# Optimization experiments

Measured on AMD Instinct MI355X. Metric: run time of the kernel, lower is better.

Reference implementation:

```python
import jax, jax.numpy as jnp
import numpy as np

ALPHA = 0.2        # LeakyReLU negative slope
MASK_VAL = -9e15   # matches torch -9000000000000000.0


def setup_inputs() -> dict:
    key = jax.random.key(0)
    k_h, k_adj, k_w, k_a = jax.random.split(key, 4)
    B, N, Nodes, IF, OF = 8, 8, 512, 256, 256
    h = jax.random.normal(k_h, (B, N, Nodes, IF), dtype=jnp.float32)
    adj = jax.random.randint(k_adj, (Nodes, Nodes), 0, 2, dtype=jnp.int32)
    # xavier_uniform with gain=1.414
    gain = 1.414
    lim_w = gain * np.sqrt(6.0 / (IF + OF))
    W = jax.random.uniform(k_w, (IF, OF), dtype=jnp.float32, minval=-lim_w, maxval=lim_w)
    lim_a = gain * np.sqrt(6.0 / (2 * OF + 1))
    a = jax.random.uniform(k_a, (2 * OF, 1), dtype=jnp.float32, minval=-lim_a, maxval=lim_a)
    return {"h": h, "adj": adj, "W": W, "a": a}


def reference(h, adj, W, a):
    # Wh: [B, N, Nodes, OF]
    Wh = jnp.matmul(h, W)
    OF = W.shape[1]
    a1, a2 = a[:OF, 0], a[OF:, 0]
    # e[..., i, j] = leakyrelu(a1 . Wh_i + a2 . Wh_j)  (decomposed additive attention)
    src = jnp.einsum('bnif,f->bni', Wh, a1)  # [B, N, Nodes]
    dst = jnp.einsum('bnjf,f->bnj', Wh, a2)  # [B, N, Nodes]
    e = jax.nn.leaky_relu(src[..., :, None] + dst[..., None, :], negative_slope=ALPHA)
    attention = jnp.where(adj > 0, e, jnp.full_like(e, MASK_VAL))
    attention = jax.nn.softmax(attention, axis=-1)
    # dropout is identity in eval mode (training=False)
    h_prime = jnp.matmul(attention, Wh)  # [B, N, Nodes, OF]
    return jax.nn.elu(h_prime)  # concat=True
```

## Files before the change

kernel.cpp:

```cpp
#include <hip/hip_runtime.h>
#include <hip/hip_bf16.h>


#define ALPHA 0.2f
#define MASK_VAL -9000000000000000.0f
#define NODES 512
#define FDIM 256
#define BN 64

typedef float  f32x4 __attribute__((ext_vector_type(4)));
typedef int    i32x4 __attribute__((ext_vector_type(4)));
typedef short  s16x8 __attribute__((ext_vector_type(8)));
typedef short  s16x4 __attribute__((ext_vector_type(4)));
typedef __bf16 bf16x8 __attribute__((ext_vector_type(8)));

__device__ __forceinline__ unsigned short f2bfu(float x) {
    __hip_bfloat16 b = __float2bfloat16(x);
    unsigned short u; __builtin_memcpy(&u, &b, 2); return u;
}
__device__ __forceinline__ float bfu2f(unsigned short u) {
    unsigned int w = ((unsigned int)u) << 16; return __uint_as_float(w);
}
__device__ __forceinline__ f32x4 mfma16(s16x8 a, s16x8 b, f32x4 c) {
    return __builtin_amdgcn_mfma_f32_16x16x32_bf16(
        __builtin_bit_cast(bf16x8, a), __builtin_bit_cast(bf16x8, b), c, 0, 0, 0);
}

__device__ __forceinline__ void split8v(f32x4 v0, f32x4 v1, s16x8& hi, s16x8& lo)
{
    float x[8] = {v0[0], v0[1], v0[2], v0[3], v1[0], v1[1], v1[2], v1[3]};
    unsigned hw[4], lw[4];
    #pragma unroll
    for (int d = 0; d < 4; ++d) {
        const unsigned u0 = __float_as_uint(x[2*d]);
        const unsigned u1 = __float_as_uint(x[2*d + 1]);
        hw[d] = __builtin_amdgcn_perm(u1, u0, 0x07060302);
        const float l0 = x[2*d]     - __uint_as_float(u0 & 0xFFFF0000u);
        const float l1 = x[2*d + 1] - __uint_as_float(u1 & 0xFFFF0000u);
        lw[d] = __builtin_amdgcn_perm(__float_as_uint(l1), __float_as_uint(l0),
                                      0x07060302);
    }
    hi = __builtin_bit_cast(s16x8, *(unsigned(*)[4])hw);
    lo = __builtin_bit_cast(s16x8, *(unsigned(*)[4])lw);
}

__device__ __forceinline__ void gll16(const void* g, void* l) {
    __builtin_amdgcn_global_load_lds(
        (const __attribute__((address_space(1))) unsigned int*)g,
        (__attribute__((address_space(3))) unsigned int*)l,
        16, 0, 0);
}

__global__ __launch_bounds__(256) void detect_kernel(const unsigned short* __restrict__ hraw,
                                                     int* __restrict__ flag)
{
    const int tid = threadIdx.x;
    float m = 0.0f;
    for (int i = tid; i < 16384; i += 256) {
        unsigned int w = ((unsigned int)hraw[i]) << 16;
        float v = __uint_as_float(w);
        v = fabsf(v);
        if (!(v == v)) v = 1e30f;
        m = fmaxf(m, v);
    }
    #pragma unroll
    for (int off = 32; off >= 1; off >>= 1)
        m = fmaxf(m, __shfl_down(m, off));
    __shared__ float red[4];
    if ((tid & 63) == 0) red[tid >> 6] = m;
    __syncthreads();
    if (tid == 0) {
        float mm = fmaxf(fmaxf(red[0], red[1]), fmaxf(red[2], red[3]));
        *flag = (mm > 1e4f) ? 1 : 0;
    }
}

__global__ __launch_bounds__(256) void prep_w_kernel(
    const void* __restrict__ Wv, const int* __restrict__ flagp,
    short* __restrict__ WtHi, short* __restrict__ WtLo)
{
    const int flag = *flagp;
    __shared__ float tile[16][17];
    const int tx = threadIdx.x & 15, ty = threadIdx.x >> 4;
    const int kk = blockIdx.y * 16 + ty;
    const int f  = blockIdx.x * 16 + tx;
    float v;
    if (flag) v = ((const float*)Wv)[kk * FDIM + f];
    else      v = bfu2f(((const unsigned short*)Wv)[kk * FDIM + f]);
    tile[ty][tx] = v;
    __syncthreads();
    const float x = tile[tx][ty];
    const int fo = blockIdx.x * 16 + ty;
    const int ko = blockIdx.y * 16 + tx;
    unsigned short h = f2bfu(x);
    WtHi[fo * FDIM + ko] = (short)h;
    WtLo[fo * FDIM + ko] = (short)f2bfu(x - bfu2f(h));
}

__global__ __launch_bounds__(256, 2) void wh_gemm(
    const void* __restrict__ hv,
    const short* __restrict__ WtHi, const short* __restrict__ WtLo,
    const void* __restrict__ av, const int* __restrict__ flagp,
    short* __restrict__ WhTHi, short* __restrict__ WhTLo,
    float* __restrict__ srcv, float* __restrict__ dstv)
{
    __shared__ __align__(16) char smem[81920];

    const int flag = *flagp;
    const int blk = blockIdx.x;
    const int bn  = blk >> 3;
    const int i0  = (blk & 7) * 64;
    const size_t r0g = (size_t)blk * 64;
    const int tid = threadIdx.x;
    const int w = tid >> 6, l = tid & 63;
    const int fb = l & 15, g = l >> 4;

    const int arow = tid >> 2, asg = tid & 3;
    const int aseg = asg ^ ((arow >> 1) & 3);
    const int awr  = arow * 64 + asg * 16;

    const short* gBh[4];
    const short* gBl[4];
    int bdst[4];
    {
        const int bsg = tid & 3;
        #pragma unroll
        for (int i = 0; i < 4; ++i) {
            const int f = i * 64 + (tid >> 2);
            const int ss = bsg ^ ((f ^ (f >> 2)) & 3);
            gBh[i] = WtHi + f * FDIM + ss * 8;
            gBl[i] = WtLo + f * FDIM + ss * 8;
            bdst[i] = (i * 256 + tid) * 16;
        }
    }

    f32x4 acc[4][4];
    #pragma unroll
    for (int rt = 0; rt < 4; ++rt)
        #pragma unroll
        for (int ct = 0; ct < 4; ++ct) acc[rt][ct] = f32x4{0.f,0.f,0.f,0.f};

    if (flag) {
        const float* gA = (const float*)hv + (r0g + arow) * FDIM + aseg * 8;
        {
            f32x4 v0 = *(const f32x4*)gA;
            f32x4 v1 = *(const f32x4*)(gA + 4);
            #pragma unroll
            for (int i = 0; i < 4; ++i) {
                gll16(gBh[i], smem + 16384 + bdst[i]);
                gll16(gBl[i], smem + 49152 + bdst[i]);
            }
            s16x8 hi, lo; split8v(v0, v1, hi, lo);
            *(s16x8*)(smem + awr) = hi;
            *(s16x8*)(smem + 4096 + awr) = lo;
        }
        __syncthreads();
        for (int t = 0; t < 8; ++t) {
            const int cur = t & 1, nxt = cur ^ 1;
            f32x4 v0 = {}, v1 = {};
            if (t < 7) {
                v0 = *(const f32x4*)(gA + (t+1)*32);
                v1 = *(const f32x4*)(gA + (t+1)*32 + 4);
                #pragma unroll
                for (int i = 0; i < 4; ++i) {
                    gll16(gBh[i] + (t+1)*32, smem + 16384 + nxt*16384 + bdst[i]);
                    gll16(gBl[i] + (t+1)*32, smem + 49152 + nxt*16384 + bdst[i]);
                }
            }
            s16x8 bh[4], bl[4], ah[4], al[4];
            #pragma unroll
            for (int ct = 0; ct < 4; ++ct) {
                const int f = w*64 + ct*16 + fb;
                const int slot = g ^ ((f ^ (f >> 2)) & 3);
                const int off = 16384 + cur*16384 + f*64 + slot*16;
                bh[ct] = *(const s16x8*)(smem + off);
                bl[ct] = *(const s16x8*)(smem + off + 32768);
            }
            #pragma unroll
            for (int rt = 0; rt < 4; ++rt) {
                const int row = rt*16 + fb;
                const int slot = g ^ ((row >> 1) & 3);
                const int off = cur*8192 + row*64 + slot*16;
                ah[rt] = *(const s16x8*)(smem + off);
                al[rt] = *(const s16x8*)(smem + off + 4096);
            }
            __builtin_amdgcn_s_setprio(1);
            #pragma unroll
            for (int rt = 0; rt < 4; ++rt)
                #pragma unroll
                for (int ct = 0; ct < 4; ++ct) {
                    acc[rt][ct] = mfma16(ah[rt], bh[ct], acc[rt][ct]);
                    acc[rt][ct] = mfma16(al[rt], bh[ct], acc[rt][ct]);
                    acc[rt][ct] = mfma16(ah[rt], bl[ct], acc[rt][ct]);
                }
            __builtin_amdgcn_s_setprio(0);
            if (t < 7) {
                s16x8 hi, lo; split8v(v0, v1, hi, lo);
                *(s16x8*)(smem + nxt*8192 + awr) = hi;
                *(s16x8*)(smem + nxt*8192 + 4096 + awr) = lo;
            }
            __syncthreads();
        }
    } else {
        const short* gA = (const short*)hv + (r0g + arow) * FDIM + aseg * 8;
        {
            s16x8 a0 = *(const s16x8*)gA;
            #pragma unroll
            for (int i = 0; i < 4; ++i) gll16(gBh[i], smem + 16384 + bdst[i]);
            *(s16x8*)(smem + awr) = a0;
        }
        __syncthreads();
        for (int t = 0; t < 8; ++t) {
            const int cur = t & 1, nxt = cur ^ 1;
            s16x8 an = {};
            if (t < 7) {
                an = *(const s16x8*)(gA + (t+1)*32);
                #pragma unroll
                for (int i = 0; i < 4; ++i)
                    gll16(gBh[i] + (t+1)*32, smem + 16384 + nxt*16384 + bdst[i]);
            }
            s16x8 bh[4], ah[4];
            #pragma unroll
            for (int ct = 0; ct < 4; ++ct) {
                const int f = w*64 + ct*16 + fb;
                const int slot = g ^ ((f ^ (f >> 2)) & 3);
                bh[ct] = *(const s16x8*)(smem + 16384 + cur*16384 + f*64 + slot*16);
            }
            #pragma unroll
            for (int rt = 0; rt < 4; ++rt) {
                const int row = rt*16 + fb;
                const int slot = g ^ ((row >> 1) & 3);
                ah[rt] = *(const s16x8*)(smem + cur*8192 + row*64 + slot*16);
            }
            __builtin_amdgcn_s_setprio(1);
            #pragma unroll
            for (int rt = 0; rt < 4; ++rt)
                #pragma unroll
                for (int ct = 0; ct < 4; ++ct)
                    acc[rt][ct] = mfma16(ah[rt], bh[ct], acc[rt][ct]);
            __builtin_amdgcn_s_setprio(0);
            if (t < 7) *(s16x8*)(smem + nxt*8192 + awr) = an;
            __syncthreads();
        }
    }

    const size_t wbT = (size_t)bn * FDIM * NODES;
    #pragma unroll
    for (int rt = 0; rt < 4; ++rt) {
        const int orow = i0 + rt * 16 + g * 4;
        #pragma unroll
        for (int ct = 0; ct < 4; ++ct) {
            const int f = w * 64 + ct * 16 + fb;
            s16x4 h4, l4;
            #pragma unroll
            for (int r = 0; r < 4; ++r) {
                float x = acc[rt][ct][r];
                unsigned short hh = f2bfu(x);
                h4[r] = (short)hh;
                l4[r] = (short)f2bfu(x - bfu2f(hh));
            }
            *(s16x4*)(WhTHi + wbT + (size_t)f * NODES + orow) = h4;
            *(s16x4*)(WhTLo + wbT + (size_t)f * NODES + orow) = l4;
        }
    }

    float a1v[4], a2v[4];
    #pragma unroll
    for (int ct = 0; ct < 4; ++ct) {
        const int f = w * 64 + ct * 16 + fb;
        if (flag) {
            a1v[ct] = ((const float*)av)[f];
            a2v[ct] = ((const float*)av)[FDIM + f];
        } else {
            a1v[ct] = bfu2f(((const unsigned short*)av)[f]);
            a2v[ct] = bfu2f(((const unsigned short*)av)[FDIM + f]);
        }
    }
    float* red1 = (float*)smem;
    float* red2 = red1 + 256;
    #pragma unroll
    for (int rt = 0; rt < 4; ++rt) {
        #pragma unroll
        for (int r = 0; r < 4; ++r) {
            float s1 = 0.f, s2 = 0.f;
            #pragma unroll
            for (int ct = 0; ct < 4; ++ct) {
                s1 = fmaf(acc[rt][ct][r], a1v[ct], s1);
                s2 = fmaf(acc[rt][ct][r], a2v[ct], s2);
            }
            #pragma unroll
            for (int off = 1; off <= 8; off <<= 1) {
                s1 += __shfl_xor(s1, off);
                s2 += __shfl_xor(s2, off);
            }
            if (fb == 0) {
                red1[w * 64 + rt * 16 + g * 4 + r] = s1;
                red2[w * 64 + rt * 16 + g * 4 + r] = s2;
            }
        }
    }
    __syncthreads();
    if (tid < 64) {
        srcv[bn * NODES + i0 + tid] =
            red1[tid] + red1[64 + tid] + red1[128 + tid] + red1[192 + tid];
        dstv[bn * NODES + i0 + tid] =
            red2[tid] + red2[64 + tid] + red2[128 + tid] + red2[192 + tid];
    }
}

__global__ __launch_bounds__(1024, 4) void pv_gemm(
    const short* __restrict__ WhTHi, const short* __restrict__ WhTLo,
    const float* __restrict__ srcv, const float* __restrict__ dstv,
    const int* __restrict__ adj, const int* __restrict__ flagp,
    void* __restrict__ out)
{
    __shared__ __align__(16) char smem[163840];

    const int flag = *flagp;
    const int b0 = blockIdx.x;
    const int blk = (b0 & 7) * 64 + (b0 >> 3);
    const int bn  = blk >> 3;
    const int i0  = (blk & 7) * 64;
    const int tid = threadIdx.x;
    const int w = tid >> 6, l = tid & 63;

    const short* bhig = WhTHi + (size_t)bn * FDIM * NODES;
    const short* blog = WhTLo + (size_t)bn * FDIM * NODES;

    const int sf = tid >> 2, ssg = tid & 3;
    const int sss = ssg ^ ((sf ^ (sf >> 2)) & 3);
    const short* gH = bhig + (size_t)sf * NODES + sss * 8;
    const short* gL = blog + (size_t)sf * NODES + sss * 8;
    char* ldsH = smem + 65536 + tid * 16;
    char* ldsL = smem + 65536 + 16384 + tid * 16;

    gll16(gH,      ldsH);          gll16(gL,      ldsL);
    gll16(gH + 32, ldsH + 32768);  gll16(gL + 32, ldsL + 32768);

    {
        const float* drow = dstv + bn * NODES;
        const int j = l * 8;
        #pragma unroll
        for (int rr = 0; rr < 4; ++rr) {
            const int r = w * 4 + rr;
            const int* adjrow = adj + (size_t)(i0 + r) * NODES;
            const float srow = srcv[bn * NODES + i0 + r];
            const i32x4 q0 = *(const i32x4*)(adjrow + j);
            const i32x4 q1 = *(const i32x4*)(adjrow + j + 4);
            const f32x4 d0 = *(const f32x4*)(drow + j);
            const f32x4 d1 = *(const f32x4*)(drow + j + 4);
            float e[8];
            #pragma unroll
            for (int k = 0; k < 4; ++k) {
                float ev = srow + d0[k];
                ev = (ev > 0.f) ? ev : ALPHA * ev;
                e[k] = (q0[k] > 0) ? ev : MASK_VAL;
                float ew = srow + d1[k];
                ew = (ew > 0.f) ? ew : ALPHA * ew;
                e[4 + k] = (q1[k] > 0) ? ew : MASK_VAL;
            }
            float m = e[0];
            #pragma unroll
            for (int k = 1; k < 8; ++k) m = fmaxf(m, e[k]);
            #pragma unroll
            for (int off = 1; off <= 32; off <<= 1) m = fmaxf(m, __shfl_xor(m, off));
            float p[8], s = 0.f;
            #pragma unroll
            for (int k = 0; k < 8; ++k) {
                p[k] = __expf(e[k] - m);
                s += p[k];
            }
            #pragma unroll
            for (int off = 1; off <= 32; off <<= 1) s += __shfl_xor(s, off);
            const float isum = 1.0f / s;
            s16x8 ph;
            #pragma unroll
            for (int k = 0; k < 8; ++k) ph[k] = (short)f2bfu(p[k] * isum);
            *(s16x8*)(smem + r * 1024 + ((l ^ (r & 7)) * 16)) = ph;
        }
    }
    __syncthreads();

    const int fb = l & 15, g = l >> 4;
    const int wr = w >> 2, wc = w & 3;
    const int arow = wr * 16 + fb;
    const unsigned abase = (unsigned)(arow * 1024);
    const unsigned aswz  = (unsigned)((arow & 7) << 4);

    f32x4 acc[4];
    #pragma unroll
    for (int ct = 0; ct < 4; ++ct) acc[ct] = f32x4{0.f, 0.f, 0.f, 0.f};

    unsigned boff[4];
    #pragma unroll
    for (int ct = 0; ct < 4; ++ct) {
        const int f = wc * 64 + ct * 16 + fb;
        const int slot = g ^ ((f ^ (f >> 2)) & 3);
        boff[ct] = (unsigned)(65536 + f * 64 + slot * 16);
    }

    int cur = 0;
    for (int t = 0; t < 16; ++t) {
        if (t < 15) asm volatile("s_waitcnt vmcnt(2)" ::: "memory");
        else        asm volatile("s_waitcnt vmcnt(0)" ::: "memory");
        __builtin_amdgcn_s_barrier();
        __builtin_amdgcn_sched_barrier(0);
        asm volatile("" ::: "memory");
        if (t < 14) {
            int nb = cur + 2; if (nb >= 3) nb -= 3;
            gll16(gH + (t + 2) * 32, ldsH + nb * 32768);
            gll16(gL + (t + 2) * 32, ldsL + nb * 32768);
        }
        s16x8 bh[4], bl[4];
        #pragma unroll
        for (int ct = 0; ct < 4; ++ct) {
            const unsigned off = boff[ct] + (unsigned)(cur * 32768);
            bh[ct] = *(const s16x8*)(smem + off);
            bl[ct] = *(const s16x8*)(smem + off + 16384);
        }
        const unsigned aoff = abase + ((((unsigned)(t * 4 + g)) * 16) ^ aswz);
        const s16x8 a = *(const s16x8*)(smem + aoff);
        __builtin_amdgcn_s_setprio(1);
        #pragma unroll
        for (int ct = 0; ct < 4; ++ct) {
            acc[ct] = mfma16(a, bh[ct], acc[ct]);
            acc[ct] = mfma16(a, bl[ct], acc[ct]);
        }
        __builtin_amdgcn_s_setprio(0);
        cur = cur + 1; if (cur == 3) cur = 0;
    }

    #pragma unroll
    for (int ct = 0; ct < 4; ++ct) {
        const int f = wc * 64 + ct * 16 + fb;
        #pragma unroll
        for (int r = 0; r < 4; ++r) {
            float v = acc[ct][r];
            v = (v > 0.f) ? v : expm1f(v);
            const size_t o = ((size_t)bn * NODES + i0 + wr * 16 + g * 4 + r) * FDIM + f;
            if (flag) ((float*)out)[o] = v;
            else      ((unsigned short*)out)[o] = f2bfu(v);
        }
    }
}

extern "C" void kernel_launch(void* const* d_in, const int* in_sizes, int n_in,
                              void* d_out, int out_size, void* d_ws, size_t ws_size,
                              hipStream_t stream)
{
    const void* h   = d_in[0];
    const int*  adj = (const int*)d_in[1];
    const void* W   = d_in[2];
    const void* a   = d_in[3];

    int*   flag  = (int*)d_ws;
    float* srcv  = (float*)d_ws + 64;
    float* dstv  = srcv + BN * NODES;
    short* WtHi  = (short*)(dstv + BN * NODES);
    short* WtLo  = WtHi + FDIM * FDIM;
    short* WhTHi = WtLo + FDIM * FDIM;
    short* WhTLo = WhTHi + (size_t)BN * FDIM * NODES;

    detect_kernel<<<1, 256, 0, stream>>>((const unsigned short*)h, flag);
    prep_w_kernel<<<dim3(16, 16), 256, 0, stream>>>(W, flag, WtHi, WtLo);
    wh_gemm<<<512, 256, 0, stream>>>(h, WtHi, WtLo, a, flag,
                                     WhTHi, WhTLo, srcv, dstv);
    pv_gemm<<<512, 1024, 0, stream>>>(WhTHi, WhTLo, srcv, dstv, adj, flag, d_out);
}
```

Before: 164.1 us.

## Retile pv_gemm to 512 threads with wave-private B tiles and no loop barriers

The attention-times-Wh kernel goes from 1024 to 512 threads per block. Each wave now computes a 64x32 output tile instead of 16x64, so it reads four A fragments and two B fragment pairs per k-step, which improves register-level reuse. Each wave stages only its own 32 feature rows of Wh into LDS, so the per-iteration block barrier is replaced by per-wave vmcnt/lgkmcnt waits. The softmax row loop now covers 8 rows per wave. The cost is more accumulator registers per thread and fewer waves to hide latency. A swizzle macro is also introduced as cleanup.

```diff
diff --git a/kernel.cpp b/kernel.cpp
--- a/kernel.cpp
+++ b/kernel.cpp
@@ -7,6 +7,7 @@
 #define NODES 512
 #define FDIM 256
 #define BN 64
+#define SWZ(f) ((((f) ^ ((f) >> 2))) & 3)
 
 typedef float  f32x4 __attribute__((ext_vector_type(4)));
 typedef int    i32x4 __attribute__((ext_vector_type(4)));
@@ -127,7 +128,7 @@
         #pragma unroll
         for (int i = 0; i < 4; ++i) {
             const int f = i * 64 + (tid >> 2);
-            const int ss = bsg ^ ((f ^ (f >> 2)) & 3);
+            const int ss = bsg ^ SWZ(f);
             gBh[i] = WtHi + f * FDIM + ss * 8;
             gBl[i] = WtLo + f * FDIM + ss * 8;
             bdst[i] = (i * 256 + tid) * 16;
@@ -171,7 +172,7 @@
             #pragma unroll
             for (int ct = 0; ct < 4; ++ct) {
                 const int f = w*64 + ct*16 + fb;
-                const int slot = g ^ ((f ^ (f >> 2)) & 3);
+                const int slot = g ^ SWZ(f);
                 const int off = 16384 + cur*16384 + f*64 + slot*16;
                 bh[ct] = *(const s16x8*)(smem + off);
                 bl[ct] = *(const s16x8*)(smem + off + 32768);
@@ -223,7 +224,7 @@
             #pragma unroll
             for (int ct = 0; ct < 4; ++ct) {
                 const int f = w*64 + ct*16 + fb;
-                const int slot = g ^ ((f ^ (f >> 2)) & 3);
+                const int slot = g ^ SWZ(f);
                 bh[ct] = *(const s16x8*)(smem + 16384 + cur*16384 + f*64 + slot*16);
             }
             #pragma unroll
@@ -308,7 +309,7 @@
     }
 }
 
-__global__ __launch_bounds__(1024, 4) void pv_gemm(
+__global__ __launch_bounds__(512, 2) void pv_gemm(
     const short* __restrict__ WhTHi, const short* __restrict__ WhTLo,
     const float* __restrict__ srcv, const float* __restrict__ dstv,
     const int* __restrict__ adj, const int* __restrict__ flagp,
@@ -327,22 +328,32 @@
     const short* bhig = WhTHi + (size_t)bn * FDIM * NODES;
     const short* blog = WhTLo + (size_t)bn * FDIM * NODES;
 
-    const int sf = tid >> 2, ssg = tid & 3;
-    const int sss = ssg ^ ((sf ^ (sf >> 2)) & 3);
-    const short* gH = bhig + (size_t)sf * NODES + sss * 8;
-    const short* gL = blog + (size_t)sf * NODES + sss * 8;
-    char* ldsH = smem + 65536 + tid * 16;
-    char* ldsL = smem + 65536 + 16384 + tid * 16;
-
-    gll16(gH,      ldsH);          gll16(gL,      ldsL);
-    gll16(gH + 32, ldsH + 32768);  gll16(gL + 32, ldsL + 32768);
+    const int sf0 = w * 32 + (l >> 2);
+    const int sf1 = sf0 + 16;
+    const int sl  = l & 3;
+    const short* gH0 = bhig + (size_t)sf0 * NODES + (sl ^ SWZ(sf0)) * 8;
+    const short* gH1 = bhig + (size_t)sf1 * NODES + (sl ^ SWZ(sf1)) * 8;
+    const short* gL0 = blog + (size_t)sf0 * NODES + (sl ^ SWZ(sf0)) * 8;
+    const short* gL1 = blog + (size_t)sf1 * NODES + (sl ^ SWZ(sf1)) * 8;
+    const int dB = (w * 32) * 64 + l * 16;
+
+    auto stage = [&](int buf, int t) {
+        const int ko = t * 32;
+        char* base = smem + 65536 + buf * 32768;
+        gll16(gH0 + ko, base + dB);
+        gll16(gH1 + ko, base + dB + 1024);
+        gll16(gL0 + ko, base + 16384 + dB);
+        gll16(gL1 + ko, base + 16384 + dB + 1024);
+    };
+
+    stage(0, 0);
+    stage(1, 1);
 
     {
         const float* drow = dstv + bn * NODES;
         const int j = l * 8;
-        #pragma unroll
-        for (int rr = 0; rr < 4; ++rr) {
-            const int r = w * 4 + rr;
+        for (int rr = 0; rr < 8; ++rr) {
+            const int r = w * 8 + rr;
             const int* adjrow = adj + (size_t)(i0 + r) * NODES;
             const float srow = srcv[bn * NODES + i0 + r];
             const i32x4 q0 = *(const i32x4*)(adjrow + j);
@@ -379,67 +390,78 @@
             *(s16x8*)(smem + r * 1024 + ((l ^ (r & 7)) * 16)) = ph;
         }
     }
-    __syncthreads();
+    asm volatile("s_waitcnt lgkmcnt(0)" ::: "memory");
+    __builtin_amdgcn_s_barrier();
 
     const int fb = l & 15, g = l >> 4;
-    const int wr = w >> 2, wc = w & 3;
-    const int arow = wr * 16 + fb;
-    const unsigned abase = (unsigned)(arow * 1024);
-    const unsigned aswz  = (unsigned)((arow & 7) << 4);
-
-    f32x4 acc[4];
-    #pragma unroll
-    for (int ct = 0; ct < 4; ++ct) acc[ct] = f32x4{0.f, 0.f, 0.f, 0.f};
-
-    unsigned boff[4];
-    #pragma unroll
-    for (int ct = 0; ct < 4; ++ct) {
-        const int f = wc * 64 + ct * 16 + fb;
-        const int slot = g ^ ((f ^ (f >> 2)) & 3);
-        boff[ct] = (unsigned)(65536 + f * 64 + slot * 16);
-    }
+
+    unsigned boff[2];
+    #pragma unroll
+    for (int ct = 0; ct < 2; ++ct) {
+        const int f = w * 32 + ct * 16 + fb;
+        boff[ct] = (unsigned)(65536 + f * 64 + (g ^ SWZ(f)) * 16);
+    }
+    unsigned aoff[4];
+    #pragma unroll
+    for (int rt = 0; rt < 4; ++rt) {
+        const int row = rt * 16 + fb;
+        aoff[rt] = (unsigned)(row * 1024) | 0x80000000u * 0u;
+    }
+
+    f32x4 acc[4][2];
+    #pragma unroll
+    for (int rt = 0; rt < 4; ++rt)
+        #pragma unroll
+        for (int ct = 0; ct < 2; ++ct) acc[rt][ct] = f32x4{0.f,0.f,0.f,0.f};
 
     int cur = 0;
     for (int t = 0; t < 16; ++t) {
-        if (t < 15) asm volatile("s_waitcnt vmcnt(2)" ::: "memory");
+        if (t < 15) asm volatile("s_waitcnt vmcnt(4)" ::: "memory");
         else        asm volatile("s_waitcnt vmcnt(0)" ::: "memory");
-        __builtin_amdgcn_s_barrier();
-        __builtin_amdgcn_sched_barrier(0);
-        asm volatile("" ::: "memory");
         if (t < 14) {
             int nb = cur + 2; if (nb >= 3) nb -= 3;
-            gll16(gH + (t + 2) * 32, ldsH + nb * 32768);
-            gll16(gL + (t + 2) * 32, ldsL + nb * 32768);
-        }
-        s16x8 bh[4], bl[4];
-        #pragma unroll
-        for (int ct = 0; ct < 4; ++ct) {
-            const unsigned off = boff[ct] + (unsigned)(cur * 32768);
-            bh[ct] = *(const s16x8*)(smem + off);
-            bl[ct] = *(const s16x8*)(smem + off + 16384);
-        }
-        const unsigned aoff = abase + ((((unsigned)(t * 4 + g)) * 16) ^ aswz);
-        const s16x8 a = *(const s16x8*)(smem + aoff);
+            asm volatile("s_waitcnt lgkmcnt(0)" ::: "memory");
+            stage(nb, t + 2);
+        }
+        const unsigned bbase = (unsigned)(cur * 32768);
+        s16x8 bh[2], bl[2];
+        #pragma unroll
+        for (int ct = 0; ct < 2; ++ct) {
+            bh[ct] = *(const s16x8*)(smem + bbase + boff[ct]);
+            bl[ct] = *(const s16x8*)(smem + bbase + boff[ct] + 16384);
+        }
+        s16x8 af[4];
+        #pragma unroll
+        for (int rt = 0; rt < 4; ++rt) {
+            const int row = rt * 16 + fb;
+            const unsigned seg = (unsigned)(t * 4 + g) ^ (unsigned)(row & 7);
+            af[rt] = *(const s16x8*)(smem + aoff[rt] + seg * 16);
+        }
         __builtin_amdgcn_s_setprio(1);
         #pragma unroll
-        for (int ct = 0; ct < 4; ++ct) {
-            acc[ct] = mfma16(a, bh[ct], acc[ct]);
-            acc[ct] = mfma16(a, bl[ct], acc[ct]);
+        for (int rt = 0; rt < 4; ++rt) {
+            acc[rt][0] = mfma16(af[rt], bh[0], acc[rt][0]);
+            acc[rt][0] = mfma16(af[rt], bl[0], acc[rt][0]);
+            acc[rt][1] = mfma16(af[rt], bh[1], acc[rt][1]);
+            acc[rt][1] = mfma16(af[rt], bl[1], acc[rt][1]);
         }
         __builtin_amdgcn_s_setprio(0);
         cur = cur + 1; if (cur == 3) cur = 0;
     }
 
     #pragma unroll
-    for (int ct = 0; ct < 4; ++ct) {
-        const int f = wc * 64 + ct * 16 + fb;
-        #pragma unroll
-        for (int r = 0; r < 4; ++r) {
-            float v = acc[ct][r];
-            v = (v > 0.f) ? v : expm1f(v);
-            const size_t o = ((size_t)bn * NODES + i0 + wr * 16 + g * 4 + r) * FDIM + f;
-            if (flag) ((float*)out)[o] = v;
-            else      ((unsigned short*)out)[o] = f2bfu(v);
+    for (int rt = 0; rt < 4; ++rt) {
+        #pragma unroll
+        for (int ct = 0; ct < 2; ++ct) {
+            const int f = w * 32 + ct * 16 + fb;
+            #pragma unroll
+            for (int r = 0; r < 4; ++r) {
+                float v = acc[rt][ct][r];
+                v = (v > 0.f) ? v : expm1f(v);
+                const size_t o = ((size_t)bn * NODES + i0 + rt * 16 + g * 4 + r) * FDIM + f;
+                if (flag) ((float*)out)[o] = v;
+                else      ((unsigned short*)out)[o] = f2bfu(v);
+            }
         }
     }
 }
@@ -465,5 +487,5 @@
     prep_w_kernel<<<dim3(16, 16), 256, 0, stream>>>(W, flag, WtHi, WtLo);
     wh_gemm<<<512, 256, 0, stream>>>(h, WtHi, WtLo, a, flag,
                                      WhTHi, WhTLo, srcv, dstv);
-    pv_gemm<<<512, 1024, 0, stream>>>(WhTHi, WhTLo, srcv, dstv, adj, flag, d_out);
-}
+    pv_gemm<<<512, 512, 0, stream>>>(WhTHi, WhTLo, srcv, dstv, adj, flag, d_out);
+}
```

Measured after the change: 171.9 us. 1.05x slower.
